# Performance work log

Measured on AMD Instinct MI355X. Metric: run time of the kernel, lower is better.

## Reference

```python
import jax, jax.numpy as jnp
import numpy as np

Q = 3  # q_order: SelfONN concatenates powers x^1..x^Q on channel dim

def selfonn_conv(x, w, b, pad):
    # x: (B, C, H, W); w: (O, C*Q, kh, kw); b: (O,)
    xp = jnp.concatenate([x ** (i + 1) for i in range(Q)], axis=1)
    y = jax.lax.conv_general_dilated(
        xp, w, window_strides=(1, 1), padding=[(pad, pad), (pad, pad)],
        dimension_numbers=("NCHW", "OIHW", "NCHW"))
    return y + b[None, :, None, None]

def setup_inputs() -> dict:
    key = jax.random.key(0)
    ks = jax.random.split(key, 9)
    B, C, H, W = 4, 64, 64, 64
    P = 64  # pab_channels
    s1 = 1.0 / np.sqrt(C * Q)          # 1x1 convs
    s3 = 1.0 / np.sqrt(C * Q * 9)      # 3x3 convs
    return {
        "x": jax.random.normal(ks[0], (B, C, H, W), jnp.float32),
        "top_w": jax.random.normal(ks[1], (P, C * Q, 1, 1), jnp.float32) * s1,
        "top_b": jnp.zeros((P,), jnp.float32),
        "center_w": jax.random.normal(ks[2], (P, C * Q, 1, 1), jnp.float32) * s1,
        "center_b": jnp.zeros((P,), jnp.float32),
        "bottom_w": jax.random.normal(ks[3], (C, C * Q, 3, 3), jnp.float32) * s3,
        "bottom_b": jnp.zeros((C,), jnp.float32),
        "out_w": jax.random.normal(ks[4], (C, C * Q, 3, 3), jnp.float32) * s3,
        "out_b": jnp.zeros((C,), jnp.float32),
    }

def reference(x, top_w, top_b, center_w, center_b, bottom_w, bottom_b, out_w, out_b):
    B, C, H, W = x.shape
    HW = H * W
    x_top = selfonn_conv(x, top_w, top_b, 0).reshape(B, -1, HW)            # (B, P, HW)
    x_center = selfonn_conv(x, center_w, center_b, 0).reshape(B, -1, HW)  # (B, P, HW)
    x_bottom = selfonn_conv(x, bottom_w, bottom_b, 1).reshape(B, C, HW)   # (B, C, HW)
    x_center = jnp.swapaxes(x_center, 1, 2)  # (B, HW, P)
    x_bottom = jnp.swapaxes(x_bottom, 1, 2)  # (B, HW, C)
    sp = jnp.einsum("bnp,bpm->bnm", x_center, x_top)  # (B, HW, HW)
    # GLOBAL softmax over the entire HW*HW map per sample (dim=1 on flattened view)
    sp = jax.nn.softmax(sp.reshape(B, -1), axis=1).reshape(B, HW, HW)
    sp = jnp.einsum("bnm,bmc->bnc", sp, x_bottom)  # (B, HW, C)
    # faithful to torch: raw reshape (B, HW, C) -> (B, C, H, W), no transpose
    sp = sp.reshape(B, C, H, W)
    return selfonn_conv(x + sp, out_w, out_b, 1)
```

## Files before the change

### kernel.cpp

```cpp
#include <hip/hip_runtime.h>
#include <hip/hip_bf16.h>

namespace {
constexpr int IMG    = 262144;
constexpr int PADIMG = 4356;
constexpr float LOG2E = 1.44269504088896340736f;
constexpr int WBFO  = 0;
constexpr int XPADO = 122880;
constexpr int TOPO  = 1795584;
constexpr int CENO  = 2319872;
constexpr int BOTO  = 2844160;
constexpr int PVO   = 3368448;
constexpr int MSO4  = 5465600;
constexpr int MSO8  = 7562752;
constexpr size_t NEED8 = (size_t)(MSO8 + 8192) * 4;
}

using half8v  = __attribute__((ext_vector_type(8))) _Float16;
using half4v  = __attribute__((ext_vector_type(4))) _Float16;
using short8v = __attribute__((ext_vector_type(8))) short;
using short4v = __attribute__((ext_vector_type(4))) short;
using uint4v  = __attribute__((ext_vector_type(4))) unsigned;
typedef __attribute__((ext_vector_type(4))) float f32x4;

__device__ __forceinline__ short f2bf(float f) {
    __hip_bfloat16 h = __float2bfloat16(f);
    return *reinterpret_cast<short*>(&h);
}
__device__ __forceinline__ float bf2f(short s) {
    unsigned u = ((unsigned)(unsigned short)s) << 16;
    return __uint_as_float(u);
}
__device__ __forceinline__ unsigned pkrtz(float a, float b) {
    return __builtin_bit_cast(unsigned, __builtin_amdgcn_cvt_pkrtz(a, b));
}

__global__ __launch_bounds__(256) void k_prep(const float* __restrict__ bw, const float* __restrict__ ow,
                                              const float* __restrict__ tw, const float* __restrict__ cw,
                                              _Float16* __restrict__ wbf,
                                              const float* __restrict__ x, _Float16* __restrict__ xpad) {
    __shared__ float xs[64 * 65];
    int bx = blockIdx.x, t = threadIdx.x;
    if (bx < 960) {
        int idx = bx * 256 + t;
        if (idx < 221184) {
            int tsel = idx / 110592;
            int r    = idx - tsel * 110592;
            int tap  = r / 12288;
            int rr   = r - tap * 12288;
            int ck   = rr / 2048;
            int r2   = rr - ck * 2048;
            int o    = r2 >> 5;
            int ki   = r2 & 31;
            int k    = ck * 32 + ki;
            int p    = k >> 6, ci = k & 63;
            const float* src = tsel ? ow : bw;
            wbf[idx] = (_Float16)src[o * 1728 + (p * 64 + ci) * 9 + tap];
        } else {
            int j = idx - 221184;
            int tsel = j / 12288;
            int rr   = j - tsel * 12288;
            int ck   = rr / 2048;
            int r2   = rr - ck * 2048;
            int o    = r2 >> 5;
            int ki   = r2 & 31;
            int k    = ck * 32 + ki;
            wbf[idx] = (_Float16)(tsel ? cw[o * 192 + k] * LOG2E : tw[o * 192 + k]);
        }
        return;
    }
    int bx2 = bx - 960;
    int b = bx2 >> 6, h = bx2 & 63;
    {
        _Float16* base = xpad + (size_t)b * 6 * PADIMG * 32;
        int px[6];
        px[0] = (h + 1) * 66;
        px[1] = (h + 1) * 66 + 65;
        px[2] = h;
        px[3] = 65 * 66 + h;
        int npx = 4;
        if (h < 2) { px[4] = 64 + h; px[5] = 65 * 66 + 64 + h; npx = 6; }
        int pi = t / 24, ck = t % 24;
        if (pi < npx) {
            int cp = ck >> 2, q = ck & 3;
            half8v z = {0, 0, 0, 0, 0, 0, 0, 0};
            *(half8v*)&base[((size_t)cp * PADIMG + px[pi]) * 32 + q * 8] = z;
        }
    }
    #pragma unroll
    for (int it = 0; it < 16; ++it) {
        int idx = it * 256 + t;
        int ci = idx >> 6, wc = idx & 63;
        xs[ci * 65 + wc] = x[b * IMG + ci * 4096 + h * 64 + wc];
    }
    __syncthreads();
    _Float16* dst = xpad + ((size_t)b * 6 * PADIMG + (h + 1) * 66 + 1) * 32;
    #pragma unroll
    for (int it = 0; it < 6; ++it) {
        int u = it * 256 + t;
        int ck = u >> 8, within = u & 255;
        int px = within >> 2, q = within & 3;
        int k0 = ck * 32 + q * 8;
        int p = k0 >> 6, c0 = k0 & 63;
        half8v o;
        #pragma unroll
        for (int j = 0; j < 8; ++j) {
            float v = xs[(c0 + j) * 65 + px];
            float pw = (p == 0) ? v : ((p == 1) ? v * v : v * v * v);
            o[j] = (_Float16)pw;
        }
        *(half8v*)&dst[((size_t)ck * PADIMG + px) * 32 + q * 8] = o;
    }
}

__device__ __forceinline__ void conv3d32(int bx, int t,
                                         const _Float16* __restrict__ src,
                                         const _Float16* __restrict__ wt,
                                         const float* __restrict__ bias,
                                         _Float16* __restrict__ dh_, float* __restrict__ df) {
    int lane = t & 63, w = t >> 6;
    int l16 = lane & 15, quad = lane >> 4;
    int oh = bx >> 8, mt = bx & 255;
    int b = mt >> 6, h = mt & 63;
    const _Float16* abase = src + ((size_t)b * 6 * PADIMG + (h + 1) * 66 + 1 + w * 16 + l16) * 32 + quad * 8;
    const _Float16* bbase = wt + (size_t)(oh * 32 + l16) * 32 + quad * 8;
    f32x4 acc[2];
    acc[0] = (f32x4){0.f, 0.f, 0.f, 0.f};
    acc[1] = (f32x4){0.f, 0.f, 0.f, 0.f};
    for (int tap = 0; tap < 9; ++tap) {
        int dh = tap / 3 - 1, dw = tap % 3 - 1;
        const _Float16* arow = abase + (dh * 66 + dw) * 32;
        const _Float16* brow = bbase + (size_t)tap * 6 * 2048;
        #pragma unroll
        for (int c6 = 0; c6 < 6; ++c6) {
            half8v afr  = *(const half8v*)&arow[(size_t)c6 * PADIMG * 32];
            half8v bfr0 = *(const half8v*)&brow[(size_t)c6 * 2048];
            half8v bfr1 = *(const half8v*)&brow[(size_t)c6 * 2048 + 512];
            acc[0] = __builtin_amdgcn_mfma_f32_16x16x32_f16(afr, bfr0, acc[0], 0, 0, 0);
            acc[1] = __builtin_amdgcn_mfma_f32_16x16x32_f16(afr, bfr1, acc[1], 0, 0, 0);
        }
    }
    #pragma unroll
    for (int nf = 0; nf < 2; ++nf) {
        int c = oh * 32 + nf * 16 + l16;
        float bv = bias[c];
        size_t oi = (size_t)b * 262144 + (size_t)c * 4096 + h * 64 + w * 16 + quad * 4;
        if (dh_) {
            half4v o;
            #pragma unroll
            for (int r = 0; r < 4; ++r) o[r] = (_Float16)(acc[nf][r] + bv);
            *(half4v*)&dh_[oi] = o;
        } else {
            float4 o = make_float4(acc[nf][0] + bv, acc[nf][1] + bv, acc[nf][2] + bv, acc[nf][3] + bv);
            *(float4*)&df[oi] = o;
        }
    }
}

__global__ __launch_bounds__(256) void k_convs(const _Float16* __restrict__ xpad,
                                               const _Float16* __restrict__ wbf,
                                               const float* __restrict__ tb, const float* __restrict__ cb,
                                               const float* __restrict__ bbias,
                                               _Float16* __restrict__ topd, _Float16* __restrict__ cend,
                                               _Float16* __restrict__ botb) {
    int bx = blockIdx.x, t = threadIdx.x;
    if (bx < 512) {
        conv3d32(bx, t, xpad, wbf , bbias, botb, nullptr);
        return;
    }
    int bx2 = bx - 512;
    int lane = t & 63, w = t >> 6;
    int l16 = lane & 15, quad = lane >> 4;
    int ot = bx2 >> 8, mt = bx2 & 255;
    int b = mt >> 6, h = mt & 63;
    const _Float16* wt   = wbf + (ot ? 233472 : 221184);
    const float*    bias = ot ? cb : tb;
    _Float16*       dst  = (ot ? cend : topd) + (size_t)b * IMG;
    const _Float16* abase = xpad + ((size_t)b * 6 * PADIMG + (h + 1) * 66 + 1 + w * 16 + l16) * 32 + quad * 8;
    const _Float16* bbase = wt + (size_t)l16 * 32 + quad * 8;
    f32x4 acc[4];
    #pragma unroll
    for (int nf = 0; nf < 4; ++nf) acc[nf] = (f32x4){0.f, 0.f, 0.f, 0.f};
    #pragma unroll
    for (int kc = 0; kc < 6; ++kc) {
        half8v afr = *(const half8v*)&abase[(size_t)kc * PADIMG * 32];
        #pragma unroll
        for (int nf = 0; nf < 4; ++nf) {
            half8v bfr = *(const half8v*)&bbase[(size_t)kc * 2048 + nf * 16 * 32];
            acc[nf] = __builtin_amdgcn_mfma_f32_16x16x32_f16(afr, bfr, acc[nf], 0, 0, 0);
        }
    }
    _Float16* dp = dst + (size_t)(h * 64 + w * 16) * 64;
    #pragma unroll
    for (int nf = 0; nf < 4; ++nf) {
        float bv = bias[nf * 16 + l16];
        if (ot) bv *= LOG2E;
        #pragma unroll
        for (int r = 0; r < 4; ++r)
            dp[(quad * 4 + r) * 64 + nf * 16 + l16] = (_Float16)(acc[nf][r] + bv);
    }
}

template<int MT>
__global__ __launch_bounds__(256, 4) void k_attn(float* __restrict__ ws, int msoOff, int zsoOff) {
    __shared__ _Float16 ltop[2][64 * 72];
    __shared__ _Float16 lbot[2][64 * 72];
    int t    = threadIdx.x;
    int lane = t & 63, w = t >> 6;
    int l16  = lane & 15, quad = lane >> 4;
    int bxr = blockIdx.x;
    int bx  = (bxr & 7) * ((int)gridDim.x >> 3) + (bxr >> 3);
    int st = bx & 31, b = (bx >> 5) & 3, s = bx >> 7;
    int n0 = st * 128;
    int mbase = s * MT * 64;
    const _Float16* topg = (const _Float16*)(ws + TOPO) + (size_t)b * IMG;
    const _Float16* ceng = (const _Float16*)(ws + CENO) + (size_t)b * IMG;
    const _Float16* botg = (const _Float16*)(ws + BOTO) + (size_t)b * IMG;

    half8v bcen[2][2];
    #pragma unroll
    for (int nj = 0; nj < 2; ++nj)
        #pragma unroll
        for (int kk = 0; kk < 2; ++kk)
            bcen[nj][kk] = *(const half8v*)&ceng[(size_t)(n0 + w * 32 + nj * 16 + l16) * 64 + kk * 32 + quad * 8];

    int r0 = t >> 3, r1 = r0 + 32, off = (t & 7) * 8;

    f32x4 pv[4][2];
    #pragma unroll
    for (int cj = 0; cj < 4; ++cj)
        #pragma unroll
        for (int nj = 0; nj < 2; ++nj) pv[cj][nj] = (f32x4){0.f, 0.f, 0.f, 0.f};
    float runm = -3.0e38f, zacc = 0.f;

    half8v rt0 = *(const half8v*)&topg[(size_t)(mbase + r0) * 64 + off];
    half8v rt1 = *(const half8v*)&topg[(size_t)(mbase + r1) * 64 + off];
    half8v rb0 = *(const half8v*)&botg[(size_t)r0 * 4096 + mbase + off];
    half8v rb1 = *(const half8v*)&botg[(size_t)r1 * 4096 + mbase + off];

    #pragma unroll
    for (int tt = 0; tt < MT; ++tt) {
        _Float16* lt = ltop[tt & 1];
        _Float16* lb = lbot[tt & 1];
        *(half8v*)&lt[r0 * 72 + off] = rt0;
        *(half8v*)&lt[r1 * 72 + off] = rt1;
        *(half8v*)&lb[r0 * 72 + off] = rb0;
        *(half8v*)&lb[r1 * 72 + off] = rb1;
        __syncthreads();
        if (tt + 1 < MT) {
            int m1 = mbase + (tt + 1) * 64;
            rt0 = *(const half8v*)&topg[(size_t)(m1 + r0) * 64 + off];
            rt1 = *(const half8v*)&topg[(size_t)(m1 + r1) * 64 + off];
            rb0 = *(const half8v*)&botg[(size_t)r0 * 4096 + m1 + off];
            rb1 = *(const half8v*)&botg[(size_t)r1 * 4096 + m1 + off];
        }
        f32x4 sa[4][2];
        #pragma unroll
        for (int mi = 0; mi < 4; ++mi)
            #pragma unroll
            for (int nj = 0; nj < 2; ++nj) sa[mi][nj] = (f32x4){0.f, 0.f, 0.f, 0.f};
        __builtin_amdgcn_s_setprio(1);
        #pragma unroll
        for (int kk = 0; kk < 2; ++kk)
            #pragma unroll
            for (int mi = 0; mi < 4; ++mi) {
                half8v at = *(half8v*)&lt[(mi * 16 + l16) * 72 + kk * 32 + quad * 8];
                sa[mi][0] = __builtin_amdgcn_mfma_f32_16x16x32_f16(at, bcen[0][kk], sa[mi][0], 0, 0, 0);
                sa[mi][1] = __builtin_amdgcn_mfma_f32_16x16x32_f16(at, bcen[1][kk], sa[mi][1], 0, 0, 0);
            }
        __builtin_amdgcn_s_setprio(0);
        float lm = -3.0e38f;
        #pragma unroll
        for (int mi = 0; mi < 4; ++mi)
            #pragma unroll
            for (int nj = 0; nj < 2; ++nj) {
                float a  = fmaxf(sa[mi][nj][0], sa[mi][nj][1]);
                float c2 = fmaxf(sa[mi][nj][2], sa[mi][nj][3]);
                lm = fmaxf(lm, fmaxf(a, c2));
            }
        if (!__all(lm - runm <= 8.0f)) {
            float tm = lm;
            for (int o2 = 32; o2; o2 >>= 1) tm = fmaxf(tm, __shfl_xor(tm, o2, 64));
            if (tm > runm) {
                float sc = __builtin_amdgcn_exp2f(runm - tm);
                zacc *= sc;
                #pragma unroll
                for (int cj = 0; cj < 4; ++cj)
                    #pragma unroll
                    for (int nj = 0; nj < 2; ++nj) pv[cj][nj] *= sc;
                runm = tm;
            }
        }
        #pragma unroll
        for (int kb = 0; kb < 2; ++kb) {
            unsigned pk[2][2][2];
            #pragma unroll
            for (int f = 0; f < 2; ++f) {
                int mi = 2 * kb + f;
                #pragma unroll
                for (int nj = 0; nj < 2; ++nj) {
                    float e0 = __builtin_amdgcn_exp2f(sa[mi][nj][0] - runm);
                    float e1 = __builtin_amdgcn_exp2f(sa[mi][nj][1] - runm);
                    float e2 = __builtin_amdgcn_exp2f(sa[mi][nj][2] - runm);
                    float e3 = __builtin_amdgcn_exp2f(sa[mi][nj][3] - runm);
                    zacc += (e0 + e1) + (e2 + e3);
                    pk[f][nj][0] = pkrtz(e0, e1);
                    pk[f][nj][1] = pkrtz(e2, e3);
                }
            }
            half8v pa[2];
            #pragma unroll
            for (int nj = 0; nj < 2; ++nj) {
                unsigned T[4];
                #pragma unroll
                for (int d = 0; d < 2; ++d) {
                    unsigned X = pk[0][nj][d], Y = pk[1][nj][d];
                    asm("v_permlane32_swap_b32 %0, %1" : "+v"(X), "+v"(Y));
                    asm("v_permlane16_swap_b32 %0, %1" : "+v"(X), "+v"(Y));
                    T[d]     = X;
                    T[d + 2] = Y;
                }
                uint4v tv = {T[0], T[1], T[2], T[3]};
                pa[nj] = __builtin_bit_cast(half8v, tv);
            }
            __builtin_amdgcn_s_setprio(1);
            #pragma unroll
            for (int cj = 0; cj < 4; ++cj) {
                half8v ab = *(half8v*)&lb[(cj * 16 + l16) * 72 + kb * 32 + quad * 8];
                pv[cj][0] = __builtin_amdgcn_mfma_f32_16x16x32_f16(ab, pa[0], pv[cj][0], 0, 0, 0);
                pv[cj][1] = __builtin_amdgcn_mfma_f32_16x16x32_f16(ab, pa[1], pv[cj][1], 0, 0, 0);
            }
            __builtin_amdgcn_s_setprio(0);
        }
    }
    for (int o2 = 32; o2; o2 >>= 1) zacc += __shfl_xor(zacc, o2, 64);
    if (lane == 0) {
        ws[msoOff + s * 512 + b * 128 + st * 4 + w] = runm;
        ws[zsoOff + s * 512 + b * 128 + st * 4 + w] = zacc;
    }
    short* pvp = (short*)(ws + PVO) + (size_t)s * 1048576 + (size_t)b * IMG;
    #pragma unroll
    for (int cj = 0; cj < 4; ++cj)
        #pragma unroll
        for (int nj = 0; nj < 2; ++nj) {
            short4v o;
            #pragma unroll
            for (int r = 0; r < 4; ++r) o[r] = f2bf(pv[cj][nj][r]);
            *(short4v*)&pvp[(size_t)(n0 + w * 32 + nj * 16 + l16) * 64 + cj * 16 + quad * 4] = o;
        }
}

__global__ __launch_bounds__(512) void k_finalu(const float* __restrict__ x, float* __restrict__ ws,
                                                _Float16* __restrict__ upad,
                                                int ms, int msoOff, int zsoOff) {
    __shared__ float us[64 * 65];
    __shared__ float rm[8], rz[8];
    int t = threadIdx.x, bx = blockIdx.x;
    int b = bx >> 6, h = bx & 63;
    int g = t & 127;
    float m = -3.0e38f;
    for (int s = 0; s < ms; ++s)
        m = fmaxf(m, ws[msoOff + s * 512 + b * 128 + g]);
    for (int o2 = 32; o2; o2 >>= 1) m = fmaxf(m, __shfl_xor(m, o2, 64));
    if ((t & 63) == 0) rm[t >> 6] = m;
    __syncthreads();
    float M = rm[0];
    #pragma unroll
    for (int j = 1; j < 8; ++j) M = fmaxf(M, rm[j]);
    float z = 0.f;
    if (t < 128) {
        for (int s = 0; s < ms; ++s)
            z += ws[zsoOff + s * 512 + b * 128 + g] *
                 __builtin_amdgcn_exp2f(ws[msoOff + s * 512 + b * 128 + g] - M);
    }
    for (int o2 = 32; o2; o2 >>= 1) z += __shfl_xor(z, o2, 64);
    if ((t & 63) == 0) rz[t >> 6] = z;
    __syncthreads();
    float Z = 0.f;
    #pragma unroll
    for (int j = 0; j < 8; ++j) Z += rz[j];
    float rZ = 1.0f / Z;

    const short* pvb = (const short*)(ws + PVO) + (size_t)b * IMG;
    int hg = h >> 5;
    {
        int idx = t * 8;
        int ci = idx >> 6, wc = idx & 63;
        int rem = ci * 4096 + h * 64 + wc;
        int grp = ci * 2 + hg;
        float acc[8] = {};
        for (int s = 0; s < ms; ++s) {
            float scl = __builtin_amdgcn_exp2f(ws[msoOff + s * 512 + b * 128 + grp] - M);
            short8v pvv = *(const short8v*)&pvb[(size_t)s * 1048576 + rem];
            #pragma unroll
            for (int i = 0; i < 8; ++i) acc[i] += bf2f(pvv[i]) * scl;
        }
        float4 x0 = *(const float4*)&x[(size_t)b * IMG + rem];
        float4 x1 = *(const float4*)&x[(size_t)b * IMG + rem + 4];
        float xv[8] = {x0.x, x0.y, x0.z, x0.w, x1.x, x1.y, x1.z, x1.w};
        #pragma unroll
        for (int i = 0; i < 8; ++i)
            us[ci * 65 + wc + i] = xv[i] + acc[i] * rZ;
    }
    __syncthreads();
    _Float16* dst = upad + ((size_t)b * 6 * PADIMG + (h + 1) * 66 + 1) * 32;
    #pragma unroll
    for (int it = 0; it < 3; ++it) {
        int u = it * 512 + t;
        int ck = u >> 8, within = u & 255;
        int px = within >> 2, q = within & 3;
        int k0 = ck * 32 + q * 8;
        int p = k0 >> 6, c0 = k0 & 63;
        half8v o;
        #pragma unroll
        for (int j = 0; j < 8; ++j) {
            float v = us[(c0 + j) * 65 + px];
            float pw = (p == 0) ? v : ((p == 1) ? v * v : v * v * v);
            o[j] = (_Float16)pw;
        }
        *(half8v*)&dst[((size_t)ck * PADIMG + px) * 32 + q * 8] = o;
    }
}

__global__ __launch_bounds__(256) void k_conv3o(const _Float16* __restrict__ upad,
                                                const _Float16* __restrict__ wout,
                                                const float* __restrict__ ob,
                                                float* __restrict__ out) {
    conv3d32(blockIdx.x, threadIdx.x, upad, wout, ob, nullptr, out);
}

extern "C" void kernel_launch(void* const* d_in, const int* in_sizes, int n_in,
                              void* d_out, int out_size, void* d_ws, size_t ws_size,
                              hipStream_t stream) {
    (void)in_sizes; (void)n_in; (void)out_size;
    const float* x  = (const float*)d_in[0];
    const float* tw = (const float*)d_in[1];
    const float* tb = (const float*)d_in[2];
    const float* cw = (const float*)d_in[3];
    const float* cb = (const float*)d_in[4];
    const float* bw = (const float*)d_in[5];
    const float* bb = (const float*)d_in[6];
    const float* ow = (const float*)d_in[7];
    const float* ob = (const float*)d_in[8];
    float* ws  = (float*)d_ws;
    float* out = (float*)d_out;

    _Float16* wbf  = (_Float16*)(ws + WBFO);
    _Float16* wout = wbf + 110592;
    _Float16* xpad = (_Float16*)(ws + XPADO);
    _Float16* topb = (_Float16*)(ws + TOPO);
    _Float16* cenb = (_Float16*)(ws + CENO);
    _Float16* botb = (_Float16*)(ws + BOTO);

    int ms     = (ws_size >= NEED8) ? 8 : 4;
    int msoOff = (ms == 8) ? MSO8 : MSO4;
    int zsoOff = msoOff + ms * 512;

    hipLaunchKernelGGL(k_prep, dim3(1216), dim3(256), 0, stream, bw, ow, tw, cw, wbf, x, xpad);
    hipLaunchKernelGGL(k_convs, dim3(1024), dim3(256), 0, stream, xpad, wbf, tb, cb, bb, topb, cenb, botb);
    if (ms == 8)
        hipLaunchKernelGGL(k_attn<8>,  dim3(1024), dim3(256), 0, stream, ws, msoOff, zsoOff);
    else
        hipLaunchKernelGGL(k_attn<16>, dim3(512),  dim3(256), 0, stream, ws, msoOff, zsoOff);
    hipLaunchKernelGGL(k_finalu, dim3(256), dim3(512), 0, stream, x, ws, xpad, ms, msoOff, zsoOff);
    hipLaunchKernelGGL(k_conv3o, dim3(512), dim3(256), 0, stream, xpad, wout, ob, out);
}
```

Before: 159.1 us.

## Stage attention tiles with direct global-to-LDS loads and XOR-swizzled layout

Replaces the register-staged global loads and LDS stores in the attention kernel with global_load_lds transfers that write straight into shared memory. The padded 72-stride layout becomes an unpadded 64-stride layout with an XOR swizzle to avoid bank conflicts, which cuts VGPR pressure and LDS footprint. The bottom-conv tap loop is also fully unrolled. The risk is that there is only one barrier per iteration while async loads into the other buffer may race with reads from the previous iteration, since no explicit vmcnt wait is visible before the barrier.

```diff
diff --git a/kernel.cpp b/kernel.cpp
--- a/kernel.cpp
+++ b/kernel.cpp
@@ -33,6 +33,11 @@
 }
 __device__ __forceinline__ unsigned pkrtz(float a, float b) {
     return __builtin_bit_cast(unsigned, __builtin_amdgcn_cvt_pkrtz(a, b));
+}
+__device__ __forceinline__ void gload16(const void* g, void* l) {
+    __builtin_amdgcn_global_load_lds(
+        (const __attribute__((address_space(1))) unsigned*)g,
+        (__attribute__((address_space(3))) unsigned*)l, 16, 0, 0);
 }
 
 __global__ __launch_bounds__(256) void k_prep(const float* __restrict__ bw, const float* __restrict__ ow,
@@ -127,6 +132,7 @@
     f32x4 acc[2];
     acc[0] = (f32x4){0.f, 0.f, 0.f, 0.f};
     acc[1] = (f32x4){0.f, 0.f, 0.f, 0.f};
+    #pragma unroll
     for (int tap = 0; tap < 9; ++tap) {
         int dh = tap / 3 - 1, dw = tap % 3 - 1;
         const _Float16* arow = abase + (dh * 66 + dw) * 32;
@@ -203,8 +209,8 @@
 
 template<int MT>
 __global__ __launch_bounds__(256, 4) void k_attn(float* __restrict__ ws, int msoOff, int zsoOff) {
-    __shared__ _Float16 ltop[2][64 * 72];
-    __shared__ _Float16 lbot[2][64 * 72];
+    __shared__ _Float16 ltop[2][64 * 64];
+    __shared__ _Float16 lbot[2][64 * 64];
     int t    = threadIdx.x;
     int lane = t & 63, w = t >> 6;
     int l16  = lane & 15, quad = lane >> 4;
@@ -217,6 +223,17 @@
     const _Float16* ceng = (const _Float16*)(ws + CENO) + (size_t)b * IMG;
     const _Float16* botg = (const _Float16*)(ws + BOTO) + (size_t)b * IMG;
 
+    int r0   = t >> 3;
+    int swz0 = ((t & 7) ^ (r0 & 7)) * 8;
+    int rsw  = (l16 & 7) * 8;
+
+    auto stage = [&](int buf, int mt) {
+        gload16(topg + (size_t)(mt + r0) * 64 + swz0,      &ltop[buf][w * 512]);
+        gload16(topg + (size_t)(mt + r0 + 32) * 64 + swz0, &ltop[buf][2048 + w * 512]);
+        gload16(botg + (size_t)r0 * 4096 + mt + swz0,      &lbot[buf][w * 512]);
+        gload16(botg + (size_t)(r0 + 32) * 4096 + mt + swz0, &lbot[buf][2048 + w * 512]);
+    };
+
     half8v bcen[2][2];
     #pragma unroll
     for (int nj = 0; nj < 2; ++nj)
@@ -224,8 +241,6 @@
         for (int kk = 0; kk < 2; ++kk)
             bcen[nj][kk] = *(const half8v*)&ceng[(size_t)(n0 + w * 32 + nj * 16 + l16) * 64 + kk * 32 + quad * 8];
 
-    int r0 = t >> 3, r1 = r0 + 32, off = (t & 7) * 8;
-
     f32x4 pv[4][2];
     #pragma unroll
     for (int cj = 0; cj < 4; ++cj)
@@ -233,27 +248,14 @@
         for (int nj = 0; nj < 2; ++nj) pv[cj][nj] = (f32x4){0.f, 0.f, 0.f, 0.f};
     float runm = -3.0e38f, zacc = 0.f;
 
-    half8v rt0 = *(const half8v*)&topg[(size_t)(mbase + r0) * 64 + off];
-    half8v rt1 = *(const half8v*)&topg[(size_t)(mbase + r1) * 64 + off];
-    half8v rb0 = *(const half8v*)&botg[(size_t)r0 * 4096 + mbase + off];
-    half8v rb1 = *(const half8v*)&botg[(size_t)r1 * 4096 + mbase + off];
+    stage(0, mbase);
 
     #pragma unroll
     for (int tt = 0; tt < MT; ++tt) {
-        _Float16* lt = ltop[tt & 1];
-        _Float16* lb = lbot[tt & 1];
-        *(half8v*)&lt[r0 * 72 + off] = rt0;
-        *(half8v*)&lt[r1 * 72 + off] = rt1;
-        *(half8v*)&lb[r0 * 72 + off] = rb0;
-        *(half8v*)&lb[r1 * 72 + off] = rb1;
+        const _Float16* lt = ltop[tt & 1];
+        const _Float16* lb = lbot[tt & 1];
         __syncthreads();
-        if (tt + 1 < MT) {
-            int m1 = mbase + (tt + 1) * 64;
-            rt0 = *(const half8v*)&topg[(size_t)(m1 + r0) * 64 + off];
-            rt1 = *(const half8v*)&topg[(size_t)(m1 + r1) * 64 + off];
-            rb0 = *(const half8v*)&botg[(size_t)r0 * 4096 + m1 + off];
-            rb1 = *(const half8v*)&botg[(size_t)r1 * 4096 + m1 + off];
-        }
+        if (tt + 1 < MT) stage((tt + 1) & 1, mbase + (tt + 1) * 64);
         f32x4 sa[4][2];
         #pragma unroll
         for (int mi = 0; mi < 4; ++mi)
@@ -264,7 +266,7 @@
         for (int kk = 0; kk < 2; ++kk)
             #pragma unroll
             for (int mi = 0; mi < 4; ++mi) {
-                half8v at = *(half8v*)&lt[(mi * 16 + l16) * 72 + kk * 32 + quad * 8];
+                half8v at = *(half8v*)&lt[(mi * 16 + l16) * 64 + ((kk * 32 + quad * 8) ^ rsw)];
                 sa[mi][0] = __builtin_amdgcn_mfma_f32_16x16x32_f16(at, bcen[0][kk], sa[mi][0], 0, 0, 0);
                 sa[mi][1] = __builtin_amdgcn_mfma_f32_16x16x32_f16(at, bcen[1][kk], sa[mi][1], 0, 0, 0);
             }
@@ -326,7 +328,7 @@
             __builtin_amdgcn_s_setprio(1);
             #pragma unroll
             for (int cj = 0; cj < 4; ++cj) {
-                half8v ab = *(half8v*)&lb[(cj * 16 + l16) * 72 + kb * 32 + quad * 8];
+                half8v ab = *(half8v*)&lb[(cj * 16 + l16) * 64 + ((kb * 32 + quad * 8) ^ rsw)];
                 pv[cj][0] = __builtin_amdgcn_mfma_f32_16x16x32_f16(ab, pa[0], pv[cj][0], 0, 0, 0);
                 pv[cj][1] = __builtin_amdgcn_mfma_f32_16x16x32_f16(ab, pa[1], pv[cj][1], 0, 0, 0);
             }
```

New measurement: 159.6 us. No clear change (+0.3%).
